# Kernel tuning notes

Measured on AMD Instinct MI355X. Metric: run time of the kernel, lower is better.

Reference implementation:

```python
import jax, jax.numpy as jnp
import numpy as np

N = 1024
BATCH = 16384


def setup_inputs() -> dict:
    key = jax.random.key(0)
    k1, k2 = jax.random.split(key)
    log_alpha = jax.random.normal(k1, (BATCH, N), dtype=jnp.float32)
    W = jax.random.normal(k2, (N, N), dtype=jnp.float32)  # unnormalized_transition_matrix
    return {"log_alpha": log_alpha, "W": W}


def reference(log_alpha, W):
    # log_softmax over dim=0 (columns sum to 1 in prob space)
    logT = jax.nn.log_softmax(W, axis=0)  # [N, N]
    # log-domain matmul: out[b, i] = logsumexp_k( logT[i, k] + log_alpha[b, k] )
    # Stable exp-shift trick avoids materializing the [B, N, N] broadcast tensor:
    mA = jnp.max(logT, axis=1, keepdims=True)        # [N, 1] row max of logT
    mB = jnp.max(log_alpha, axis=1, keepdims=True)   # [B, 1] row max of log_alpha
    expA = jnp.exp(logT - mA)                        # [N, N]
    expB = jnp.exp(log_alpha - mB)                   # [B, N]
    s = jnp.einsum('bk,ik->bi', expB, expA)          # [B, N]
    return jnp.log(s) + mB + mA.T                    # [B, N]
```

## Files before the change

### kernel.cpp

```cpp
#include <hip/hip_runtime.h>
#include <hip/hip_bf16.h>
#include <stdint.h>

#define MB_ 16384
#define NN_ 1024
#define KK_ 1024

typedef __bf16 bhalf;
typedef __bf16 bhalf8 __attribute__((ext_vector_type(8)));
typedef __bf16 bhalf4 __attribute__((ext_vector_type(4)));
typedef float f32x4 __attribute__((ext_vector_type(4)));

typedef const __attribute__((address_space(1))) void* gas_ptr;
typedef __attribute__((address_space(3))) void* las_ptr;

__device__ __forceinline__ void gload_lds16(const void* g, void* l) {
  __builtin_amdgcn_global_load_lds((gas_ptr)g, (las_ptr)l, 16, 0, 0);
}

__global__ void k_colpart(const float* __restrict__ W,
                          float* __restrict__ pM, float* __restrict__ pS) {
  int col = blockIdx.x * 256 + threadIdx.x;
  int rc  = blockIdx.y;
  const float* p = W + (size_t)rc * 32 * NN_ + col;
  float v[32];
#pragma unroll
  for (int i = 0; i < 32; ++i) v[i] = p[(size_t)i * NN_];
  float m = v[0];
#pragma unroll
  for (int i = 1; i < 32; ++i) m = fmaxf(m, v[i]);
  float s = 0.f;
#pragma unroll
  for (int i = 0; i < 32; ++i) s += __expf(v[i] - m);
  pM[rc * NN_ + col] = m;
  pS[rc * NN_ + col] = s;
}

__global__ void k_colfin(const float* __restrict__ pM, const float* __restrict__ pS,
                         float* __restrict__ colLSE) {
  int col = blockIdx.x * 256 + threadIdx.x;
  float m = -1e30f;
#pragma unroll
  for (int i = 0; i < 32; ++i) m = fmaxf(m, pM[i * NN_ + col]);
  float s = 0.f;
#pragma unroll
  for (int i = 0; i < 32; ++i) s += pS[i * NN_ + col] * __expf(pM[i * NN_ + col] - m);
  colLSE[col] = m + __logf(s);
}

__global__ void k_expA(const float* __restrict__ W, const float* __restrict__ colLSE,
                       bhalf* __restrict__ eA) {
  int i = blockIdx.x;
  int l = threadIdx.x;
  const float4* row = (const float4*)(W + (size_t)i * NN_);
  const float4* cls = (const float4*)colLSE;
#pragma unroll
  for (int t = 0; t < 4; ++t) {
    float4 wv = row[t * 64 + l];
    float4 cv = cls[t * 64 + l];
    bhalf4 o;
    o[0] = (bhalf)__expf(wv.x - cv.x);
    o[1] = (bhalf)__expf(wv.y - cv.y);
    o[2] = (bhalf)__expf(wv.z - cv.z);
    o[3] = (bhalf)__expf(wv.w - cv.w);
    *(bhalf4*)(eA + (size_t)i * NN_ + t * 256 + l * 4) = o;
  }
}


#define VMW(N)  asm volatile("s_waitcnt vmcnt(" #N ")" ::: "memory")
#define LGKM0   asm volatile("s_waitcnt lgkmcnt(0)" ::: "memory")
#define HINT8   asm volatile("s_waitcnt lgkmcnt(8)" ::: "memory")
#define SBAR    __builtin_amdgcn_s_barrier()
#define SCB0    __builtin_amdgcn_sched_barrier(0)
#define NOPS    ((void)0)

#define STB(BUF, H, TOFF) do {                                                \
    const bhalf* g_ = pgB + (H) * 131072 + (TOFF) * 64;                       \
    unsigned char* d_ = lds + 65536 + (BUF) * 32768 + (H) * 16384 + tid * 16; \
    gload_lds16(g_, d_); gload_lds16(g_ + 65536, d_ + 8192); } while (0)

#define LOADA(TOFF) do {                                                      \
    _Pragma("unroll")                                                         \
    for (int r_ = 0; r_ < 8; ++r_) va[r_] = pLA4[r_ * 8192 + (TOFF) * 16];    \
  } while (0)

#define CVTA_H(BUF, H) do {                                                   \
    unsigned char* d_ = dA_base + (BUF) * 32768 + (H) * 16384;                \
    _Pragma("unroll")                                                         \
    for (int j_ = 0; j_ < 4; ++j_) {                                          \
      float4 u_ = va[(H) * 4 + j_];                                           \
      bhalf4 o_;                                                              \
      o_[0] = (bhalf)__expf(u_.x); o_[1] = (bhalf)__expf(u_.y);               \
      o_[2] = (bhalf)__expf(u_.z); o_[3] = (bhalf)__expf(u_.w);               \
      *(bhalf4*)(d_ + j_ * 4096) = o_;                                        \
    } } while (0)

#define DS_AF(BUF, Q)                                                         \
  af[0][0] = *(const bhalf8*)(pA0 + (BUF) * 32768 + (Q) * 4096);              \
  af[0][1] = *(const bhalf8*)(pA1 + (BUF) * 32768 + (Q) * 4096);              \
  af[1][0] = *(const bhalf8*)(pA0 + (BUF) * 32768 + (Q) * 4096 + 2048);       \
  af[1][1] = *(const bhalf8*)(pA1 + (BUF) * 32768 + (Q) * 4096 + 2048);

#define DS_BQ(BUF)                                                            \
  _Pragma("unroll")                                                           \
  for (int n_ = 0; n_ < 4; ++n_) {                                            \
    bq[n_][0] = *(const bhalf8*)(pB0 + (BUF) * 32768 + n_ * 2048);            \
    bq[n_][1] = *(const bhalf8*)(pB1 + (BUF) * 32768 + n_ * 2048);            \
  }

#define MFMA8(Q)                                                              \
  __builtin_amdgcn_s_setprio(1);                                              \
  _Pragma("unroll")                                                           \
  for (int m_ = 0; m_ < 2; ++m_)                                              \
    _Pragma("unroll")                                                         \
    for (int n_ = 0; n_ < 4; ++n_)                                            \
      _Pragma("unroll")                                                       \
      for (int kk_ = 0; kk_ < 2; ++kk_)                                       \
        acc[2 * (Q) + m_][n_] = __builtin_amdgcn_mfma_f32_16x16x32_bf16(      \
            af[m_][kk_], bq[n_][kk_], acc[2 * (Q) + m_][n_], 0, 0, 0);        \
  __builtin_amdgcn_s_setprio(0);

#define HEAD  SCB0; SBAR; LGKM0; SCB0

#define KTILE(BUF, LT, BT, W1, CV)                                            \
  {                                                                           \
    bhalf8 bq[4][2];                                                          \
    bhalf8 af[2][2];                                                          \
    DS_AF(BUF, 0) DS_BQ(BUF)                                                  \
    HINT8;                                                                    \
    HEAD; MFMA8(0) SBAR;                                                      \
    DS_AF(BUF, 1)                                                             \
    if ((BT) >= 0) STB(BUF, 0, BT);                                           \
    HEAD; MFMA8(1)                                                            \
    W1;                                                                       \
    if (CV) CVTA_H((BUF) ^ 1, 0);                                             \
    SCB0; SBAR;                                                               \
    DS_AF(BUF, 2)                                                             \
    if ((BT) >= 0) STB(BUF, 1, BT);                                           \
    HEAD; MFMA8(2)                                                            \
    if (CV) CVTA_H((BUF) ^ 1, 1);                                             \
    if ((LT) >= 0) LOADA(LT);                                                 \
    SCB0; SBAR;                                                               \
    DS_AF(BUF, 3)                                                             \
    HEAD; MFMA8(3) SBAR;                                                      \
  }

__global__ __launch_bounds__(512, 2) void k_gemm(const float* __restrict__ LA,
                                                 const bhalf* __restrict__ Bt,
                                                 float* __restrict__ out) {
  __shared__ __align__(16) unsigned char lds[131072];

  const int nwg = gridDim.x;
  const int wg  = blockIdx.x;
  const int swz = (wg & 7) * (nwg >> 3) + (wg >> 3);
  const int bm = swz >> 2;
  const int bn = swz & 3;

  const int tid = threadIdx.x;
  const int l = tid & 63;
  const int w = tid >> 6;
  const int wr = w >> 2;
  const int wc = w & 3;

  const int r8  = tid >> 3;
  const int kel = (((tid & 7) ^ (r8 & 7)) << 3);
  const bhalf* pgB = Bt + (size_t)(bn * 256 + r8) * KK_ + kel;

  const float4* pLA4 = (const float4*)(LA + (size_t)(bm * 256 + (tid >> 4)) * KK_) + (tid & 15);
  unsigned char* dA_base = lds + (tid >> 4) * 128 +
                           ((((tid & 15) >> 1) ^ ((tid >> 4) & 7)) << 4) + ((tid & 1) << 3);

  const int kx  = 16 * (l >> 4);
  const int x16 = (l & 7) << 4;
  const int kx0 = kx ^ x16;
  const int kx1 = (64 + kx) ^ x16;
  const unsigned char* pA0 = lds + wr * 16384 + (l & 15) * 128 + kx0;
  const unsigned char* pA1 = lds + wr * 16384 + (l & 15) * 128 + kx1;
  const unsigned char* pB0 = lds + 65536 + (wc >> 1) * 16384 + ((wc & 1) * 64 + (l & 15)) * 128 + kx0;
  const unsigned char* pB1 = lds + 65536 + (wc >> 1) * 16384 + ((wc & 1) * 64 + (l & 15)) * 128 + kx1;

  f32x4 zero = {0.f, 0.f, 0.f, 0.f};
  f32x4 acc[8][4];
#pragma unroll
  for (int m = 0; m < 8; ++m)
#pragma unroll
    for (int n = 0; n < 4; ++n) acc[m][n] = zero;

  float4 va[8];

  LOADA(0);
  STB(0, 0, 0); STB(0, 1, 0);
  STB(1, 0, 1); STB(1, 1, 1);
  VMW(8);
  CVTA_H(0, 0); CVTA_H(0, 1);
  LOADA(1);
  VMW(12);
  LGKM0;
  SBAR;

  for (int p = 0; p < 7; ++p) {
    KTILE(0, 2, 2, VMW(2), 1)
    KTILE(1, 3, 3, VMW(2), 1)
    pLA4 += 32;
    pgB  += 128;
  }
  KTILE(0, -1, -1, VMW(0), 1)
  KTILE(1, -1, -1, NOPS, 0)

  const int c0 = bn * 256 + wc * 64 + (l & 15);
  const int r0 = bm * 256 + wr * 128 + (l >> 4) * 4;
#pragma unroll
  for (int mf = 0; mf < 8; ++mf) {
#pragma unroll
    for (int r = 0; r < 4; ++r) {
      const int row = r0 + mf * 16 + r;
      float* o = out + (size_t)row * NN_ + c0;
#pragma unroll
      for (int nf = 0; nf < 4; ++nf)
        o[nf * 16] = __logf(acc[mf][nf][r]);
    }
  }
}

extern "C" void kernel_launch(void* const* d_in, const int* in_sizes, int n_in,
                              void* d_out, int out_size, void* d_ws, size_t ws_size,
                              hipStream_t stream) {
  const float* log_alpha = (const float*)d_in[0];
  const float* W         = (const float*)d_in[1];
  float* out = (float*)d_out;

  uintptr_t ws = (uintptr_t)d_ws;
  bhalf* eA     = (bhalf*)(ws);
  float* colLSE = (float*)(ws + 2097152);
  float* pM     = (float*)(ws + 2101248);
  float* pS     = (float*)(ws + 2232320);

  k_colpart<<<dim3(4, 32), 256, 0, stream>>>(W, pM, pS);
  k_colfin<<<4, 256, 0, stream>>>(pM, pS, colLSE);
  k_expA<<<NN_, 64, 0, stream>>>(W, colLSE, eA);
  k_gemm<<<(MB_ / 256) * (NN_ / 256), 512, 0, stream>>>(log_alpha, eA, out);
}
```

Before: 60.55 us.

## Shrink GEMM tile to 128x128 with 256-thread workgroups and half LDS

Reworks the fused exp+GEMM kernel from 256x256 tiles with 8 waves and 128KB LDS to 128x128 tiles with 4 waves and 64KB LDS. The grid grows from 256 to 1024 workgroups, and each K-tile now runs two 16-MFMA phases instead of four 8-MFMA phases. The A-conversion store pattern and the B load pattern are redone for the new tile shape. The aim is better CU occupancy and load balance across the 256 CUs. The cost is lower arithmetic intensity per tile, so more global traffic for A and B.

```diff
diff --git a/kernel.cpp b/kernel.cpp
--- a/kernel.cpp
+++ b/kernel.cpp
@@ -75,143 +75,141 @@
 #define SCB0    __builtin_amdgcn_sched_barrier(0)
 #define NOPS    ((void)0)
 
-#define STB(BUF, H, TOFF) do {                                                \
-    const bhalf* g_ = pgB + (H) * 131072 + (TOFF) * 64;                       \
-    unsigned char* d_ = lds + 65536 + (BUF) * 32768 + (H) * 16384 + tid * 16; \
-    gload_lds16(g_, d_); gload_lds16(g_ + 65536, d_ + 8192); } while (0)
+#define STB(OB, TOFF) do {                                                    \
+    const bhalf* g_ = pgB + (TOFF) * 64;                                      \
+    unsigned char* d_ = lds + 32768 + (OB) * 16384 + tid * 16;                \
+    gload_lds16(g_,                 d_);                                      \
+    gload_lds16(g_ + 32 * KK_,      d_ + 4096);                               \
+    gload_lds16(g_ + 64 * KK_,      d_ + 8192);                               \
+    gload_lds16(g_ + 96 * KK_,      d_ + 12288); } while (0)
 
 #define LOADA(TOFF) do {                                                      \
     _Pragma("unroll")                                                         \
-    for (int r_ = 0; r_ < 8; ++r_) va[r_] = pLA4[r_ * 8192 + (TOFF) * 16];    \
+    for (int h_ = 0; h_ < 2; ++h_)                                            \
+      _Pragma("unroll")                                                       \
+      for (int j_ = 0; j_ < 4; ++j_)                                          \
+        va[h_ * 4 + j_] = pLA4[(TOFF) * 16 + h_ * 16384 + j_ * 4];            \
   } while (0)
 
-#define CVTA_H(BUF, H) do {                                                   \
-    unsigned char* d_ = dA_base + (BUF) * 32768 + (H) * 16384;                \
+#define CVT_H(OB, H) do {                                                     \
+    unsigned char* d_ = lds + (OB) * 16384 + (H) * 8192 + dAb;                \
     _Pragma("unroll")                                                         \
     for (int j_ = 0; j_ < 4; ++j_) {                                          \
       float4 u_ = va[(H) * 4 + j_];                                           \
       bhalf4 o_;                                                              \
       o_[0] = (bhalf)__expf(u_.x); o_[1] = (bhalf)__expf(u_.y);               \
       o_[2] = (bhalf)__expf(u_.z); o_[3] = (bhalf)__expf(u_.w);               \
-      *(bhalf4*)(d_ + j_ * 4096) = o_;                                        \
+      *(bhalf4*)(d_ + aw[j_]) = o_;                                           \
     } } while (0)
 
-#define DS_AF(BUF, Q)                                                         \
-  af[0][0] = *(const bhalf8*)(pA0 + (BUF) * 32768 + (Q) * 4096);              \
-  af[0][1] = *(const bhalf8*)(pA1 + (BUF) * 32768 + (Q) * 4096);              \
-  af[1][0] = *(const bhalf8*)(pA0 + (BUF) * 32768 + (Q) * 4096 + 2048);       \
-  af[1][1] = *(const bhalf8*)(pA1 + (BUF) * 32768 + (Q) * 4096 + 2048);
-
-#define DS_BQ(BUF)                                                            \
-  _Pragma("unroll")                                                           \
-  for (int n_ = 0; n_ < 4; ++n_) {                                            \
-    bq[n_][0] = *(const bhalf8*)(pB0 + (BUF) * 32768 + n_ * 2048);            \
-    bq[n_][1] = *(const bhalf8*)(pB1 + (BUF) * 32768 + n_ * 2048);            \
-  }
-
-#define MFMA8(Q)                                                              \
+#define MFMA16(KKI)                                                           \
   __builtin_amdgcn_s_setprio(1);                                              \
   _Pragma("unroll")                                                           \
-  for (int m_ = 0; m_ < 2; ++m_)                                              \
+  for (int m_ = 0; m_ < 4; ++m_)                                              \
     _Pragma("unroll")                                                         \
     for (int n_ = 0; n_ < 4; ++n_)                                            \
-      _Pragma("unroll")                                                       \
-      for (int kk_ = 0; kk_ < 2; ++kk_)                                       \
-        acc[2 * (Q) + m_][n_] = __builtin_amdgcn_mfma_f32_16x16x32_bf16(      \
-            af[m_][kk_], bq[n_][kk_], acc[2 * (Q) + m_][n_], 0, 0, 0);        \
+      acc[m_][n_] = __builtin_amdgcn_mfma_f32_16x16x32_bf16(                  \
+          af[m_], bq[n_][KKI], acc[m_][n_], 0, 0, 0);                         \
   __builtin_amdgcn_s_setprio(0);
 
-#define HEAD  SCB0; SBAR; LGKM0; SCB0
-
-#define KTILE(BUF, LT, BT, W1, CV)                                            \
+#define KTILE(BUF, LT, BT, W1, W2, CV)                                        \
   {                                                                           \
-    bhalf8 bq[4][2];                                                          \
-    bhalf8 af[2][2];                                                          \
-    DS_AF(BUF, 0) DS_BQ(BUF)                                                  \
+    bhalf8 af[4]; bhalf8 bq[4][2];                                            \
+    _Pragma("unroll")                                                         \
+    for (int m_ = 0; m_ < 4; ++m_)                                            \
+      af[m_] = *(const bhalf8*)(pA0 + (BUF) * 16384 + m_ * 2048);             \
+    _Pragma("unroll")                                                         \
+    for (int n_ = 0; n_ < 4; ++n_) {                                          \
+      bq[n_][0] = *(const bhalf8*)(pB0 + (BUF) * 16384 + n_ * 2048);          \
+      bq[n_][1] = *(const bhalf8*)(pB1 + (BUF) * 16384 + n_ * 2048);          \
+    }                                                                         \
     HINT8;                                                                    \
-    HEAD; MFMA8(0) SBAR;                                                      \
-    DS_AF(BUF, 1)                                                             \
-    if ((BT) >= 0) STB(BUF, 0, BT);                                           \
-    HEAD; MFMA8(1)                                                            \
+    SCB0; SBAR; LGKM0; SCB0;                                                  \
+    MFMA16(0)                                                                 \
     W1;                                                                       \
-    if (CV) CVTA_H((BUF) ^ 1, 0);                                             \
+    if (CV) CVT_H((BUF) ^ 1, 0);                                              \
     SCB0; SBAR;                                                               \
-    DS_AF(BUF, 2)                                                             \
-    if ((BT) >= 0) STB(BUF, 1, BT);                                           \
-    HEAD; MFMA8(2)                                                            \
-    if (CV) CVTA_H((BUF) ^ 1, 1);                                             \
+    _Pragma("unroll")                                                         \
+    for (int m_ = 0; m_ < 4; ++m_)                                            \
+      af[m_] = *(const bhalf8*)(pA1 + (BUF) * 16384 + m_ * 2048);             \
+    if ((BT) >= 0) STB(BUF, BT);                                              \
+    SCB0; SBAR; LGKM0; SCB0;                                                  \
+    MFMA16(1)                                                                 \
+    W2;                                                                       \
+    if (CV) CVT_H((BUF) ^ 1, 1);                                              \
     if ((LT) >= 0) LOADA(LT);                                                 \
+    LGKM0;                                                                    \
     SCB0; SBAR;                                                               \
-    DS_AF(BUF, 3)                                                             \
-    HEAD; MFMA8(3) SBAR;                                                      \
-  }
-
-__global__ __launch_bounds__(512, 2) void k_gemm(const float* __restrict__ LA,
+  }
+
+__global__ __launch_bounds__(256, 2) void k_gemm(const float* __restrict__ LA,
                                                  const bhalf* __restrict__ Bt,
                                                  float* __restrict__ out) {
-  __shared__ __align__(16) unsigned char lds[131072];
+  __shared__ __align__(16) unsigned char lds[65536];
 
   const int nwg = gridDim.x;
   const int wg  = blockIdx.x;
   const int swz = (wg & 7) * (nwg >> 3) + (wg >> 3);
-  const int bm = swz >> 2;
-  const int bn = swz & 3;
+  const int bm = swz >> 3;
+  const int bn = swz & 7;
 
   const int tid = threadIdx.x;
   const int l = tid & 63;
   const int w = tid >> 6;
-  const int wr = w >> 2;
-  const int wc = w & 3;
-
-  const int r8  = tid >> 3;
-  const int kel = (((tid & 7) ^ (r8 & 7)) << 3);
-  const bhalf* pgB = Bt + (size_t)(bn * 256 + r8) * KK_ + kel;
-
-  const float4* pLA4 = (const float4*)(LA + (size_t)(bm * 256 + (tid >> 4)) * KK_) + (tid & 15);
-  unsigned char* dA_base = lds + (tid >> 4) * 128 +
-                           ((((tid & 15) >> 1) ^ ((tid >> 4) & 7)) << 4) + ((tid & 1) << 3);
+  const int wr = w >> 1;
+  const int wc = w & 1;
+
+  const bhalf* pgB = Bt + (size_t)(bn * 128 + (tid >> 3)) * KK_ +
+                     (((tid & 7) ^ ((tid >> 3) & 7)) << 3);
+
+  const float4* pLA4 = (const float4*)(LA + (size_t)(bm * 128 + (tid >> 2)) * KK_) + (tid & 3);
+  const int dAb = (tid >> 2) * 128 + ((tid & 1) << 3);
+  int aw[4];
+#pragma unroll
+  for (int j = 0; j < 4; ++j)
+    aw[j] = (((((tid & 3) >> 1) + 2 * j) ^ ((tid >> 2) & 7)) << 4);
 
   const int kx  = 16 * (l >> 4);
   const int x16 = (l & 7) << 4;
   const int kx0 = kx ^ x16;
   const int kx1 = (64 + kx) ^ x16;
-  const unsigned char* pA0 = lds + wr * 16384 + (l & 15) * 128 + kx0;
-  const unsigned char* pA1 = lds + wr * 16384 + (l & 15) * 128 + kx1;
-  const unsigned char* pB0 = lds + 65536 + (wc >> 1) * 16384 + ((wc & 1) * 64 + (l & 15)) * 128 + kx0;
-  const unsigned char* pB1 = lds + 65536 + (wc >> 1) * 16384 + ((wc & 1) * 64 + (l & 15)) * 128 + kx1;
+  const unsigned char* pA0 = lds + (wr * 64 + (l & 15)) * 128 + kx0;
+  const unsigned char* pA1 = lds + (wr * 64 + (l & 15)) * 128 + kx1;
+  const unsigned char* pB0 = lds + 32768 + (wc * 64 + (l & 15)) * 128 + kx0;
+  const unsigned char* pB1 = lds + 32768 + (wc * 64 + (l & 15)) * 128 + kx1;
 
   f32x4 zero = {0.f, 0.f, 0.f, 0.f};
-  f32x4 acc[8][4];
-#pragma unroll
-  for (int m = 0; m < 8; ++m)
+  f32x4 acc[4][4];
+#pragma unroll
+  for (int m = 0; m < 4; ++m)
 #pragma unroll
     for (int n = 0; n < 4; ++n) acc[m][n] = zero;
 
   float4 va[8];
 
   LOADA(0);
-  STB(0, 0, 0); STB(0, 1, 0);
-  STB(1, 0, 1); STB(1, 1, 1);
-  VMW(8);
-  CVTA_H(0, 0); CVTA_H(0, 1);
+  STB(0, 0);
+  VMW(4);
+  CVT_H(0, 0); CVT_H(0, 1);
   LOADA(1);
+  STB(1, 1);
   VMW(12);
   LGKM0;
   SBAR;
 
   for (int p = 0; p < 7; ++p) {
-    KTILE(0, 2, 2, VMW(2), 1)
-    KTILE(1, 3, 3, VMW(2), 1)
+    KTILE(0, 2, 2, VMW(4), VMW(4), 1)
+    KTILE(1, 3, 3, VMW(4), VMW(4), 1)
     pLA4 += 32;
     pgB  += 128;
   }
-  KTILE(0, -1, -1, VMW(0), 1)
-  KTILE(1, -1, -1, NOPS, 0)
-
-  const int c0 = bn * 256 + wc * 64 + (l & 15);
-  const int r0 = bm * 256 + wr * 128 + (l >> 4) * 4;
-#pragma unroll
-  for (int mf = 0; mf < 8; ++mf) {
+  KTILE(0, -1, -1, VMW(4), VMW(0), 1)
+  KTILE(1, -1, -1, NOPS, NOPS, 0)
+
+  const int c0 = bn * 128 + wc * 64 + (l & 15);
+  const int r0 = bm * 128 + wr * 64 + (l >> 4) * 4;
+#pragma unroll
+  for (int mf = 0; mf < 4; ++mf) {
 #pragma unroll
     for (int r = 0; r < 4; ++r) {
       const int row = r0 + mf * 16 + r;
@@ -239,5 +237,5 @@
   k_colpart<<<dim3(4, 32), 256, 0, stream>>>(W, pM, pS);
   k_colfin<<<4, 256, 0, stream>>>(pM, pS, colLSE);
   k_expA<<<NN_, 64, 0, stream>>>(W, colLSE, eA);
-  k_gemm<<<(MB_ / 256) * (NN_ / 256), 512, 0, stream>>>(log_alpha, eA, out);
-}
+  k_gemm<<<(MB_ / 128) * (NN_ / 128), 256, 0, stream>>>(log_alpha, eA, out);
+}
```

Measured after the change: 72.08 us. 1.19x slower.
